# Performance work log

Hardware: AMD Instinct MI355X
Metric: run time of the kernel (lower is better)

## Reference

```python
import jax, jax.numpy as jnp
import numpy as np

N = 50000      # nodes
E = 400000     # edges (before self-loops)
NFEAT = 256
NHID = 64
NHEAD = 8
NOUT = 128


def gat_conv(h, src, dst, W, attn_l, attn_r, bias, n, H, D):
    """DGL GATConv (eval mode: feat_drop/attn_drop are no-ops), negative_slope=0.2."""
    feat = (h @ W).reshape(n, H, D)                      # [N,H,D]
    el = jnp.einsum('nhd,hd->nh', feat, attn_l)          # [N,H]
    er = jnp.einsum('nhd,hd->nh', feat, attn_r)          # [N,H]
    e = jax.nn.leaky_relu(el[src] + er[dst], 0.2)        # [E,H]
    # segment softmax over incoming edges of each dst node
    m = jax.ops.segment_max(e, dst, num_segments=n)      # [N,H] (every node has a self-loop)
    ex = jnp.exp(e - m[dst])
    denom = jax.ops.segment_sum(ex, dst, num_segments=n)
    a = ex / denom[dst]                                  # [E,H]
    rst = jax.ops.segment_sum(a[:, :, None] * feat[src], dst, num_segments=n)  # [N,H,D]
    return rst + bias.reshape(1, H, D)


def setup_inputs() -> dict:
    key = jax.random.key(0)
    ks = jax.random.split(key, 10)
    s = 0.1
    x = jax.random.normal(ks[0], (N, NFEAT), jnp.float32)
    edge_index = jax.random.randint(ks[1], (2, E), 0, N, dtype=jnp.int64)
    W1 = jax.random.normal(ks[2], (NFEAT, NHEAD * NHID), jnp.float32) * s
    al1 = jax.random.normal(ks[3], (NHEAD, NHID), jnp.float32) * s
    ar1 = jax.random.normal(ks[4], (NHEAD, NHID), jnp.float32) * s
    b1 = jax.random.normal(ks[5], (NHEAD * NHID,), jnp.float32) * s
    W2 = jax.random.normal(ks[6], (NHEAD * NHID, NOUT), jnp.float32) * s
    al2 = jax.random.normal(ks[7], (1, NOUT), jnp.float32) * s
    ar2 = jax.random.normal(ks[8], (1, NOUT), jnp.float32) * s
    b2 = jax.random.normal(ks[9], (NOUT,), jnp.float32) * s
    return {"x": x, "edge_index": edge_index, "W1": W1, "al1": al1, "ar1": ar1,
            "b1": b1, "W2": W2, "al2": al2, "ar2": ar2, "b2": b2}


def reference(x, edge_index, W1, al1, ar1, b1, W2, al2, ar2, b2):
    n = x.shape[0]
    loop = jnp.arange(n, dtype=edge_index.dtype)
    src = jnp.concatenate([edge_index[0], loop])  # dgl.add_self_loop
    dst = jnp.concatenate([edge_index[1], loop])
    # hidden layer (dropout is identity in eval mode)
    h = gat_conv(x, src, dst, W1, al1, ar1, b1, n, NHEAD, NHID).reshape(n, NFEAT * 2)
    h = jax.nn.elu(h)
    out = gat_conv(h, src, dst, W2, al2, ar2, b2, n, 1, NOUT).reshape(n, NOUT)
    return out
```

## Files before the change

kernel.cpp:

```cpp
#include <hip/hip_runtime.h>

#define NFEAT 256
#define NHID 64
#define NHEAD 8
#define HID1 512
#define NOUT 128

typedef unsigned short ushort_t;
typedef unsigned int uint_t;
typedef __attribute__((ext_vector_type(8))) short short8;
typedef __attribute__((ext_vector_type(4))) float floatx4;
typedef __attribute__((ext_vector_type(4))) ushort_t ushort4_t;

static __device__ __forceinline__ float bf2f(uint_t s) {
    return __uint_as_float(s << 16);
}
static __device__ __forceinline__ ushort_t f2bf(float f) {
    uint_t u = __float_as_uint(f);
    u += 0x7FFF + ((u >> 16) & 1);
    return (ushort_t)(u >> 16);
}

__global__ void k_prep(const float* __restrict__ x, ushort_t* __restrict__ xb,
                       const float* __restrict__ W1, ushort_t* __restrict__ W1t,
                       const float* __restrict__ W2, ushort_t* __restrict__ W2t,
                       const int* __restrict__ dstA, int* __restrict__ deg,
                       int n, int E, int c0, int c1, int c2) {
    int blk = blockIdx.x;
    int t = threadIdx.x;
    if (blk < c0) {
        int i = blk * 256 + t;
        floatx4 f = ((const floatx4*)x)[i];
        ushort4_t o;
        #pragma unroll
        for (int j = 0; j < 4; ++j) o[j] = f2bf(f[j]);
        ((ushort4_t*)xb)[i] = o;
    } else if (blk < c1) {
        int i = (blk - c0) * 256 + t;
        int nn = i / NFEAT, kk = i % NFEAT;
        W1t[i] = f2bf(W1[(size_t)kk * HID1 + nn]);
    } else if (blk < c2) {
        int i = (blk - c1) * 256 + t;
        int nn = i / HID1, kk = i % HID1;
        W2t[i] = f2bf(W2[(size_t)kk * NOUT + nn]);
    } else {
        int i = (blk - c2) * 256 + t;
        if (i < E + n) {
            int d = (i < E) ? dstA[i] : (i - E);
            atomicAdd(&deg[d], 1);
        }
    }
}

__global__ __launch_bounds__(1024) void k_scan(const int* __restrict__ deg, int* __restrict__ indptr, int n) {
    __shared__ int part[1024];
    int t = threadIdx.x;
    int chunk = (n + 1023) >> 10;
    int b = t * chunk;
    int e = min(b + chunk, n);
    int s = 0;
    int i = b;
    for (; i + 3 < e; i += 4)
        s += (deg[i] + deg[i + 1]) + (deg[i + 2] + deg[i + 3]);
    for (; i < e; ++i) s += deg[i];
    part[t] = s;
    __syncthreads();
    for (int off = 1; off < 1024; off <<= 1) {
        int v = (t >= off) ? part[t - off] : 0;
        __syncthreads();
        part[t] += v;
        __syncthreads();
    }
    int run = (t == 0) ? 0 : part[t - 1];
    i = b;
    for (; i + 3 < e; i += 4) {
        int d0 = deg[i], d1 = deg[i + 1], d2 = deg[i + 2], d3 = deg[i + 3];
        indptr[i] = run; run += d0;
        indptr[i + 1] = run; run += d1;
        indptr[i + 2] = run; run += d2;
        indptr[i + 3] = run; run += d3;
    }
    for (; i < e; ++i) { indptr[i] = run; run += deg[i]; }
    if (t == 1023) indptr[n] = part[1023];
}

__global__ void k_fill(const int* __restrict__ srcA, const int* __restrict__ dstA, int E, int n,
                       const int* __restrict__ indptr, int* __restrict__ cnt,
                       int* __restrict__ csr_src) {
    int i = blockIdx.x * blockDim.x + threadIdx.x;
    if (i >= E + n) return;
    int s, d;
    if (i < E) { s = srcA[i]; d = dstA[i]; } else { s = i - E; d = s; }
    int pos = indptr[d] + atomicAdd(&cnt[d], 1);
    csr_src[pos] = s;
}

__global__ __launch_bounds__(256) void k_gemm1(const ushort_t* __restrict__ A,
                                               const ushort_t* __restrict__ Bt,
                                               ushort_t* __restrict__ C,
                                               const float* __restrict__ al,
                                               const float* __restrict__ ar,
                                               float* __restrict__ el, float* __restrict__ er,
                                               int M) {
    const int N = HID1, K = NFEAT;
    __shared__ __align__(16) ushort_t As[128 * 32];
    __shared__ __align__(16) ushort_t Bs[256 * 32];
    const int t = threadIdx.x;
    const int w = t >> 6, lane = t & 63;
    const int l16 = lane & 15, quad = lane >> 4;
    const int m0 = blockIdx.y * 128, n0 = blockIdx.x * 256;
    const int r0 = (w >> 1) * 64;
    const int c0 = (w & 1) * 128;

    floatx4 acc[4][8] = {};

    const int skp = (t & 3) * 8;
    for (int k0 = 0; k0 < K; k0 += 32) {
        #pragma unroll
        for (int j = 0; j < 2; ++j) {
            int r = (j * 256 + t) >> 2;
            int gr = m0 + r; if (gr >= M) gr = M - 1;
            const ushort_t* gp = A + (size_t)gr * K + k0 + skp;
            __builtin_amdgcn_global_load_lds((const __attribute__((address_space(1))) void*)gp,
                (__attribute__((address_space(3))) void*)(As + (j * 256 + (t & ~63)) * 8), 16, 0, 0);
        }
        #pragma unroll
        for (int j = 0; j < 4; ++j) {
            int r = (j * 256 + t) >> 2;
            const ushort_t* gp = Bt + (size_t)(n0 + r) * K + k0 + skp;
            __builtin_amdgcn_global_load_lds((const __attribute__((address_space(1))) void*)gp,
                (__attribute__((address_space(3))) void*)(Bs + (j * 256 + (t & ~63)) * 8), 16, 0, 0);
        }
        __syncthreads();

        short8 af[4], bf[8];
        #pragma unroll
        for (int i = 0; i < 4; ++i)
            af[i] = *(const short8*)(As + (r0 + i * 16 + l16) * 32 + quad * 8);
        #pragma unroll
        for (int j = 0; j < 8; ++j)
            bf[j] = *(const short8*)(Bs + (c0 + j * 16 + l16) * 32 + quad * 8);
        #pragma unroll
        for (int i = 0; i < 4; ++i)
            #pragma unroll
            for (int j = 0; j < 8; ++j)
                acc[i][j] = __builtin_amdgcn_mfma_f32_16x16x32_bf16(af[i], bf[j], acc[i][j], 0, 0, 0);
        __syncthreads();
    }

    #pragma unroll
    for (int i = 0; i < 4; ++i) {
        #pragma unroll
        for (int r = 0; r < 4; ++r) {
            int row = m0 + r0 + i * 16 + quad * 4 + r;
            if (row < M) {
                #pragma unroll
                for (int j = 0; j < 8; ++j)
                    C[(size_t)row * N + n0 + c0 + j * 16 + l16] = f2bf(acc[i][j][r]);
            }
        }
    }

    float alv[8], arv[8];
    #pragma unroll
    for (int j = 0; j < 8; ++j) {
        int col = n0 + c0 + j * 16 + l16;
        alv[j] = al[col];
        arv[j] = ar[col];
    }
    int head0 = (n0 + c0) >> 6;
    #pragma unroll
    for (int i = 0; i < 4; ++i) {
        #pragma unroll
        for (int r = 0; r < 4; ++r) {
            float pa = acc[i][0][r] * alv[0] + acc[i][1][r] * alv[1]
                     + acc[i][2][r] * alv[2] + acc[i][3][r] * alv[3];
            float qa = acc[i][0][r] * arv[0] + acc[i][1][r] * arv[1]
                     + acc[i][2][r] * arv[2] + acc[i][3][r] * arv[3];
            float pb = acc[i][4][r] * alv[4] + acc[i][5][r] * alv[5]
                     + acc[i][6][r] * alv[6] + acc[i][7][r] * alv[7];
            float qb = acc[i][4][r] * arv[4] + acc[i][5][r] * arv[5]
                     + acc[i][6][r] * arv[6] + acc[i][7][r] * arv[7];
            #pragma unroll
            for (int o = 8; o > 0; o >>= 1) {
                pa += __shfl_down(pa, o);
                qa += __shfl_down(qa, o);
                pb += __shfl_down(pb, o);
                qb += __shfl_down(qb, o);
            }
            if (l16 == 0) {
                int row = m0 + r0 + i * 16 + quad * 4 + r;
                if (row < M) {
                    el[row * NHEAD + head0] = pa;
                    er[row * NHEAD + head0] = qa;
                    el[row * NHEAD + head0 + 1] = pb;
                    er[row * NHEAD + head0 + 1] = qb;
                }
            }
        }
    }
}

__global__ __launch_bounds__(256) void k_gemm2(const ushort_t* __restrict__ A,
                                               const ushort_t* __restrict__ Bt,
                                               ushort_t* __restrict__ C,
                                               const float* __restrict__ al,
                                               const float* __restrict__ ar,
                                               float* __restrict__ el, float* __restrict__ er,
                                               int M) {
    const int N = NOUT, K = HID1;
    __shared__ __align__(16) ushort_t As[64 * 32];
    __shared__ __align__(16) ushort_t Bs[128 * 32];
    __shared__ float elp[64][2], erp[64][2];
    const int t = threadIdx.x;
    const int w = t >> 6, lane = t & 63;
    const int l16 = lane & 15, quad = lane >> 4;
    const int m0 = blockIdx.y * 64;
    const int r0 = (w >> 1) * 32;
    const int c0 = (w & 1) * 64;

    floatx4 acc[2][4] = {};

    const int arow = t >> 2;
    const int skp = (t & 3) * 8;
    const int wbaseA = (t & ~63) * 8;

    for (int k0 = 0; k0 < K; k0 += 32) {
        int gr = m0 + arow; if (gr >= M) gr = M - 1;
        const ushort_t* gpa = A + (size_t)gr * K + k0 + skp;
        __builtin_amdgcn_global_load_lds((const __attribute__((address_space(1))) void*)gpa,
            (__attribute__((address_space(3))) void*)(As + wbaseA), 16, 0, 0);
        #pragma unroll
        for (int j = 0; j < 2; ++j) {
            int r = (j * 256 + t) >> 2;
            const ushort_t* gpb = Bt + (size_t)r * K + k0 + skp;
            __builtin_amdgcn_global_load_lds((const __attribute__((address_space(1))) void*)gpb,
                (__attribute__((address_space(3))) void*)(Bs + (j * 256 + (t & ~63)) * 8), 16, 0, 0);
        }
        __syncthreads();

        short8 af[2], bf[4];
        #pragma unroll
        for (int i = 0; i < 2; ++i)
            af[i] = *(const short8*)(As + (r0 + i * 16 + l16) * 32 + quad * 8);
        #pragma unroll
        for (int j = 0; j < 4; ++j)
            bf[j] = *(const short8*)(Bs + (c0 + j * 16 + l16) * 32 + quad * 8);
        #pragma unroll
        for (int i = 0; i < 2; ++i)
            #pragma unroll
            for (int j = 0; j < 4; ++j)
                acc[i][j] = __builtin_amdgcn_mfma_f32_16x16x32_bf16(af[i], bf[j], acc[i][j], 0, 0, 0);
        __syncthreads();
    }

    float alv[4], arv[4];
    #pragma unroll
    for (int j = 0; j < 4; ++j) {
        int col = c0 + j * 16 + l16;
        alv[j] = al[col];
        arv[j] = ar[col];
    }
    #pragma unroll
    for (int i = 0; i < 2; ++i) {
        #pragma unroll
        for (int r = 0; r < 4; ++r) {
            int lrow = r0 + i * 16 + quad * 4 + r;
            int row = m0 + lrow;
            if (row < M) {
                #pragma unroll
                for (int j = 0; j < 4; ++j)
                    C[(size_t)row * N + c0 + j * 16 + l16] = f2bf(acc[i][j][r]);
            }
            float p = acc[i][0][r] * alv[0] + acc[i][1][r] * alv[1]
                    + acc[i][2][r] * alv[2] + acc[i][3][r] * alv[3];
            float q = acc[i][0][r] * arv[0] + acc[i][1][r] * arv[1]
                    + acc[i][2][r] * arv[2] + acc[i][3][r] * arv[3];
            #pragma unroll
            for (int o = 8; o > 0; o >>= 1) {
                p += __shfl_down(p, o);
                q += __shfl_down(q, o);
            }
            if (l16 == 0) {
                elp[lrow][w & 1] = p;
                erp[lrow][w & 1] = q;
            }
        }
    }
    __syncthreads();
    if (t < 64) {
        int row = m0 + t;
        if (row < M) {
            el[row] = elp[t][0] + elp[t][1];
            er[row] = erp[t][0] + erp[t][1];
        }
    }
}

__global__ __launch_bounds__(256) void k_agg1(const uint_t* __restrict__ fb,
                                              const float* __restrict__ el, const float* __restrict__ er,
                                              const float* __restrict__ b1,
                                              const int* __restrict__ indptr, const int* __restrict__ csr_src,
                                              uint_t* __restrict__ h1b, int n) {
    __shared__ float wch[32 * 8];
    __shared__ int sch[32];
    int node = blockIdx.x;
    int t = threadIdx.x;
    int h = t >> 5;
    int et = t >> 3, hw = t & 7;
    int e0 = indptr[node], e1 = indptr[node + 1];
    int deg = e1 - e0;
    float erv = er[node * NHEAD + hw];
    float a0 = 0.f, a1 = 0.f, den = 0.f;

    for (int base = 0; base < deg; base += 32) {
        int cnt = min(32, deg - base);
        if (et < cnt) {
            int s = csr_src[e0 + base + et];
            if (hw == 0) sch[et] = s;
            float x = el[s * NHEAD + hw] + erv;
            x = (x > 0.f) ? x : 0.2f * x;
            wch[et * 8 + hw] = __expf(x);
        }
        __syncthreads();
        int e = 0;
        for (; e + 3 < cnt; e += 4) {
            int s0 = sch[e], s1 = sch[e + 1], s2 = sch[e + 2], s3 = sch[e + 3];
            float w0 = wch[e * 8 + h], w1 = wch[(e + 1) * 8 + h];
            float w2 = wch[(e + 2) * 8 + h], w3 = wch[(e + 3) * 8 + h];
            uint_t u0 = fb[(size_t)s0 * 256 + t];
            uint_t u1 = fb[(size_t)s1 * 256 + t];
            uint_t u2 = fb[(size_t)s2 * 256 + t];
            uint_t u3 = fb[(size_t)s3 * 256 + t];
            den += (w0 + w1) + (w2 + w3);
            a0 += w0 * bf2f(u0 & 0xFFFF) + w1 * bf2f(u1 & 0xFFFF)
                + w2 * bf2f(u2 & 0xFFFF) + w3 * bf2f(u3 & 0xFFFF);
            a1 += w0 * bf2f(u0 >> 16) + w1 * bf2f(u1 >> 16)
                + w2 * bf2f(u2 >> 16) + w3 * bf2f(u3 >> 16);
        }
        for (; e < cnt; ++e) {
            int s = sch[e];
            float ww = wch[e * 8 + h];
            uint_t u = fb[(size_t)s * 256 + t];
            den += ww;
            a0 += ww * bf2f(u & 0xFFFF);
            a1 += ww * bf2f(u >> 16);
        }
        __syncthreads();
    }

    float inv = 1.f / den;
    float v0 = a0 * inv + b1[2 * t];
    float v1 = a1 * inv + b1[2 * t + 1];
    v0 = (v0 > 0.f) ? v0 : (__expf(v0) - 1.f);
    v1 = (v1 > 0.f) ? v1 : (__expf(v1) - 1.f);
    h1b[(size_t)node * 256 + t] = (uint_t)f2bf(v0) | ((uint_t)f2bf(v1) << 16);
}

__global__ __launch_bounds__(256) void k_agg2(const uint_t* __restrict__ fb2,
                                              const float* __restrict__ el2, const float* __restrict__ er2,
                                              const float* __restrict__ b2,
                                              const int* __restrict__ indptr, const int* __restrict__ csr_src,
                                              float* __restrict__ out, int n) {
    __shared__ float wch[4][64];
    __shared__ int sch[4][64];
    int w = threadIdx.x >> 6;
    int wid = blockIdx.x * 4 + w;
    int lane = threadIdx.x & 63;
    if (wid >= n) return;
    float erv = er2[wid];
    int e0 = indptr[wid], e1 = indptr[wid + 1];
    int deg = e1 - e0;
    float a0 = 0.f, a1 = 0.f, den = 0.f;

    for (int base = 0; base < deg; base += 64) {
        int cnt = min(64, deg - base);
        if (lane < cnt) {
            int s = csr_src[e0 + base + lane];
            sch[w][lane] = s;
            float x = el2[s] + erv;
            x = (x > 0.f) ? x : 0.2f * x;
            wch[w][lane] = __expf(x);
        }
        __builtin_amdgcn_wave_barrier();
        int e = 0;
        for (; e + 3 < cnt; e += 4) {
            int s0 = sch[w][e], s1 = sch[w][e + 1], s2 = sch[w][e + 2], s3 = sch[w][e + 3];
            float w0 = wch[w][e], w1 = wch[w][e + 1], w2 = wch[w][e + 2], w3 = wch[w][e + 3];
            uint_t u0 = fb2[(size_t)s0 * 64 + lane];
            uint_t u1 = fb2[(size_t)s1 * 64 + lane];
            uint_t u2 = fb2[(size_t)s2 * 64 + lane];
            uint_t u3 = fb2[(size_t)s3 * 64 + lane];
            den += (w0 + w1) + (w2 + w3);
            a0 += w0 * bf2f(u0 & 0xFFFF) + w1 * bf2f(u1 & 0xFFFF)
                + w2 * bf2f(u2 & 0xFFFF) + w3 * bf2f(u3 & 0xFFFF);
            a1 += w0 * bf2f(u0 >> 16) + w1 * bf2f(u1 >> 16)
                + w2 * bf2f(u2 >> 16) + w3 * bf2f(u3 >> 16);
        }
        for (; e < cnt; ++e) {
            int s = sch[w][e];
            float ww = wch[w][e];
            uint_t u = fb2[(size_t)s * 64 + lane];
            den += ww;
            a0 += ww * bf2f(u & 0xFFFF);
            a1 += ww * bf2f(u >> 16);
        }
        __builtin_amdgcn_wave_barrier();
    }

    float inv = 1.f / den;
    float2 o;
    o.x = a0 * inv + b2[2 * lane];
    o.y = a1 * inv + b2[2 * lane + 1];
    ((float2*)out)[(size_t)wid * 64 + lane] = o;
}

extern "C" void kernel_launch(void* const* d_in, const int* in_sizes, int n_in,
                              void* d_out, int out_size, void* d_ws, size_t ws_size,
                              hipStream_t stream) {
    const float* x   = (const float*)d_in[0];
    const int*   ei  = (const int*)d_in[1];
    const float* W1  = (const float*)d_in[2];
    const float* al1 = (const float*)d_in[3];
    const float* ar1 = (const float*)d_in[4];
    const float* b1  = (const float*)d_in[5];
    const float* W2  = (const float*)d_in[6];
    const float* al2 = (const float*)d_in[7];
    const float* ar2 = (const float*)d_in[8];
    const float* b2  = (const float*)d_in[9];

    const int n  = in_sizes[0] / NFEAT;
    const int E  = in_sizes[1] / 2;
    const int ET = E + n;
    const int* srcA = ei;
    const int* dstA = ei + E;

    char* ws = (char*)d_ws;
    size_t off = 0;
    auto alloc = [&](size_t bytes) -> void* {
        void* p = ws + off;
        off += (bytes + 255) & ~(size_t)255;
        return p;
    };
    ushort_t* xb     = (ushort_t*)alloc((size_t)n * NFEAT * 2);
    ushort_t* feat1b = (ushort_t*)alloc((size_t)n * HID1 * 2);
    ushort_t* h1b    = (ushort_t*)alloc((size_t)n * HID1 * 2);
    ushort_t* feat2b = (ushort_t*)alloc((size_t)n * NOUT * 2);
    ushort_t* W1t    = (ushort_t*)alloc((size_t)NFEAT * HID1 * 2);
    ushort_t* W2t    = (ushort_t*)alloc((size_t)HID1 * NOUT * 2);
    float* el1 = (float*)alloc((size_t)n * NHEAD * 4);
    float* er1 = (float*)alloc((size_t)n * NHEAD * 4);
    float* el2 = (float*)alloc((size_t)n * 4);
    float* er2 = (float*)alloc((size_t)n * 4);
    int* indptr = (int*)alloc((size_t)(n + 1) * 4);
    int* deg    = (int*)alloc((size_t)2 * n * 4);
    int* cnt    = deg + n;
    int* csr    = (int*)alloc((size_t)ET * 4);

    hipMemsetAsync(deg, 0, (size_t)2 * n * 4, stream);

    const int c0 = (n * NFEAT / 4) / 256;
    const int c1 = c0 + (NFEAT * HID1) / 256;
    const int c2 = c1 + (HID1 * NOUT) / 256;
    const int c3 = c2 + (ET + 255) / 256;
    k_prep<<<c3, 256, 0, stream>>>(x, xb, W1, W1t, W2, W2t, dstA, deg, n, E, c0, c1, c2);

    k_scan<<<1, 1024, 0, stream>>>(deg, indptr, n);
    k_fill<<<(ET + 255) / 256, 256, 0, stream>>>(srcA, dstA, E, n, indptr, cnt, csr);

    k_gemm1<<<dim3(HID1 / 256, (n + 127) / 128), 256, 0, stream>>>(xb, W1t, feat1b, al1, ar1, el1, er1, n);
    k_agg1<<<n, 256, 0, stream>>>((const uint_t*)feat1b, el1, er1, b1, indptr, csr, (uint_t*)h1b, n);

    k_gemm2<<<dim3(1, (n + 63) / 64), 256, 0, stream>>>(h1b, W2t, feat2b, al2, ar2, el2, er2, n);
    k_agg2<<<(n + 3) / 4, 256, 0, stream>>>((const uint_t*)feat2b, el2, er2, b2, indptr, csr, (float*)d_out, n);
}
```

Before: 387.0 us.

## Precompute layer-1 edge attention weights during CSR fill, drop shared-memory staging in agg1

The CSR fill kernel now runs after gemm1 and also computes the exponentiated leaky-relu edge scores for all 8 heads, writing them into a CSR-ordered per-edge weight array. The layer-1 aggregation reads those weights and source indices straight from global memory, with no shared-memory staging and no __syncthreads per chunk. This removes the per-node gather-compute-barrier phase, at the cost of an extra ET*8 float buffer (about 14 MB) being written and read back, and it moves the fill kernel onto the critical path after gemm1.

```diff
diff --git a/kernel.cpp b/kernel.cpp
--- a/kernel.cpp
+++ b/kernel.cpp
@@ -84,15 +84,33 @@
     if (t == 1023) indptr[n] = part[1023];
 }
 
-__global__ void k_fill(const int* __restrict__ srcA, const int* __restrict__ dstA, int E, int n,
-                       const int* __restrict__ indptr, int* __restrict__ cnt,
-                       int* __restrict__ csr_src) {
+__global__ void k_fillw(const int* __restrict__ srcA, const int* __restrict__ dstA, int E, int n,
+                        const int* __restrict__ indptr, int* __restrict__ cnt,
+                        int* __restrict__ csr_src,
+                        const float* __restrict__ el, const float* __restrict__ er,
+                        float* __restrict__ wcsr) {
     int i = blockIdx.x * blockDim.x + threadIdx.x;
     if (i >= E + n) return;
     int s, d;
     if (i < E) { s = srcA[i]; d = dstA[i]; } else { s = i - E; d = s; }
     int pos = indptr[d] + atomicAdd(&cnt[d], 1);
     csr_src[pos] = s;
+    floatx4 el0 = *(const floatx4*)(el + (size_t)s * NHEAD);
+    floatx4 el1v = *(const floatx4*)(el + (size_t)s * NHEAD + 4);
+    floatx4 er0 = *(const floatx4*)(er + (size_t)d * NHEAD);
+    floatx4 er1v = *(const floatx4*)(er + (size_t)d * NHEAD + 4);
+    floatx4 w0, w1;
+    #pragma unroll
+    for (int h = 0; h < 4; ++h) {
+        float xa = el0[h] + er0[h];
+        xa = (xa > 0.f) ? xa : 0.2f * xa;
+        w0[h] = __expf(xa);
+        float xb2 = el1v[h] + er1v[h];
+        xb2 = (xb2 > 0.f) ? xb2 : 0.2f * xb2;
+        w1[h] = __expf(xb2);
+    }
+    *(floatx4*)(wcsr + (size_t)pos * NHEAD) = w0;
+    *(floatx4*)(wcsr + (size_t)pos * NHEAD + 4) = w1;
 }
 
 __global__ __launch_bounds__(256) void k_gemm1(const ushort_t* __restrict__ A,
@@ -297,58 +315,40 @@
     }
 }
 
-__global__ __launch_bounds__(256) void k_agg1(const uint_t* __restrict__ fb,
-                                              const float* __restrict__ el, const float* __restrict__ er,
+__global__ __launch_bounds__(256) void k_agg1(const uint_t* __restrict__ fb, const float* __restrict__ wcsr,
                                               const float* __restrict__ b1,
                                               const int* __restrict__ indptr, const int* __restrict__ csr_src,
                                               uint_t* __restrict__ h1b, int n) {
-    __shared__ float wch[32 * 8];
-    __shared__ int sch[32];
     int node = blockIdx.x;
     int t = threadIdx.x;
     int h = t >> 5;
-    int et = t >> 3, hw = t & 7;
     int e0 = indptr[node], e1 = indptr[node + 1];
-    int deg = e1 - e0;
-    float erv = er[node * NHEAD + hw];
     float a0 = 0.f, a1 = 0.f, den = 0.f;
-
-    for (int base = 0; base < deg; base += 32) {
-        int cnt = min(32, deg - base);
-        if (et < cnt) {
-            int s = csr_src[e0 + base + et];
-            if (hw == 0) sch[et] = s;
-            float x = el[s * NHEAD + hw] + erv;
-            x = (x > 0.f) ? x : 0.2f * x;
-            wch[et * 8 + hw] = __expf(x);
-        }
-        __syncthreads();
-        int e = 0;
-        for (; e + 3 < cnt; e += 4) {
-            int s0 = sch[e], s1 = sch[e + 1], s2 = sch[e + 2], s3 = sch[e + 3];
-            float w0 = wch[e * 8 + h], w1 = wch[(e + 1) * 8 + h];
-            float w2 = wch[(e + 2) * 8 + h], w3 = wch[(e + 3) * 8 + h];
-            uint_t u0 = fb[(size_t)s0 * 256 + t];
-            uint_t u1 = fb[(size_t)s1 * 256 + t];
-            uint_t u2 = fb[(size_t)s2 * 256 + t];
-            uint_t u3 = fb[(size_t)s3 * 256 + t];
-            den += (w0 + w1) + (w2 + w3);
-            a0 += w0 * bf2f(u0 & 0xFFFF) + w1 * bf2f(u1 & 0xFFFF)
-                + w2 * bf2f(u2 & 0xFFFF) + w3 * bf2f(u3 & 0xFFFF);
-            a1 += w0 * bf2f(u0 >> 16) + w1 * bf2f(u1 >> 16)
-                + w2 * bf2f(u2 >> 16) + w3 * bf2f(u3 >> 16);
-        }
-        for (; e < cnt; ++e) {
-            int s = sch[e];
-            float ww = wch[e * 8 + h];
-            uint_t u = fb[(size_t)s * 256 + t];
-            den += ww;
-            a0 += ww * bf2f(u & 0xFFFF);
-            a1 += ww * bf2f(u >> 16);
-        }
-        __syncthreads();
-    }
-
+    int e = e0;
+    for (; e + 3 < e1; e += 4) {
+        int s0 = csr_src[e], s1 = csr_src[e + 1], s2 = csr_src[e + 2], s3 = csr_src[e + 3];
+        float w0 = wcsr[(size_t)e * NHEAD + h];
+        float w1 = wcsr[(size_t)(e + 1) * NHEAD + h];
+        float w2 = wcsr[(size_t)(e + 2) * NHEAD + h];
+        float w3 = wcsr[(size_t)(e + 3) * NHEAD + h];
+        uint_t u0 = fb[(size_t)s0 * 256 + t];
+        uint_t u1 = fb[(size_t)s1 * 256 + t];
+        uint_t u2 = fb[(size_t)s2 * 256 + t];
+        uint_t u3 = fb[(size_t)s3 * 256 + t];
+        den += (w0 + w1) + (w2 + w3);
+        a0 += w0 * bf2f(u0 & 0xFFFF) + w1 * bf2f(u1 & 0xFFFF)
+            + w2 * bf2f(u2 & 0xFFFF) + w3 * bf2f(u3 & 0xFFFF);
+        a1 += w0 * bf2f(u0 >> 16) + w1 * bf2f(u1 >> 16)
+            + w2 * bf2f(u2 >> 16) + w3 * bf2f(u3 >> 16);
+    }
+    for (; e < e1; ++e) {
+        int s = csr_src[e];
+        float w = wcsr[(size_t)e * NHEAD + h];
+        uint_t u = fb[(size_t)s * 256 + t];
+        den += w;
+        a0 += w * bf2f(u & 0xFFFF);
+        a1 += w * bf2f(u >> 16);
+    }
     float inv = 1.f / den;
     float v0 = a0 * inv + b1[2 * t];
     float v1 = a1 * inv + b1[2 * t + 1];
@@ -452,6 +452,7 @@
     float* er1 = (float*)alloc((size_t)n * NHEAD * 4);
     float* el2 = (float*)alloc((size_t)n * 4);
     float* er2 = (float*)alloc((size_t)n * 4);
+    float* wcsr1 = (float*)alloc((size_t)ET * NHEAD * 4);
     int* indptr = (int*)alloc((size_t)(n + 1) * 4);
     int* deg    = (int*)alloc((size_t)2 * n * 4);
     int* cnt    = deg + n;
@@ -466,10 +467,10 @@
     k_prep<<<c3, 256, 0, stream>>>(x, xb, W1, W1t, W2, W2t, dstA, deg, n, E, c0, c1, c2);
 
     k_scan<<<1, 1024, 0, stream>>>(deg, indptr, n);
-    k_fill<<<(ET + 255) / 256, 256, 0, stream>>>(srcA, dstA, E, n, indptr, cnt, csr);
 
     k_gemm1<<<dim3(HID1 / 256, (n + 127) / 128), 256, 0, stream>>>(xb, W1t, feat1b, al1, ar1, el1, er1, n);
-    k_agg1<<<n, 256, 0, stream>>>((const uint_t*)feat1b, el1, er1, b1, indptr, csr, (uint_t*)h1b, n);
+    k_fillw<<<(ET + 255) / 256, 256, 0, stream>>>(srcA, dstA, E, n, indptr, cnt, csr, el1, er1, wcsr1);
+    k_agg1<<<n, 256, 0, stream>>>((const uint_t*)feat1b, wcsr1, b1, indptr, csr, (uint_t*)h1b, n);
 
     k_gemm2<<<dim3(1, (n + 63) / 64), 256, 0, stream>>>(h1b, W2t, feat2b, al2, ar2, el2, er2, n);
     k_agg2<<<(n + 3) / 4, 256, 0, stream>>>((const uint_t*)feat2b, el2, er2, b2, indptr, csr, (float*)d_out, n);
```

After: 384.2 us. No clear change (-0.7%).
